# Kernel tuning notes

Measured on AMD Instinct MI355X. Metric: run time of the kernel, lower is better.

Reference implementation:

```python
import jax, jax.numpy as jnp
import numpy as np

ACT_BITS = 8
NUM_HEADS = 6


def weight_quant(w):
    # BitNet b1.58 absmean ternary quantization with straight-through estimator
    scale = 1.0 / jnp.maximum(jnp.mean(jnp.abs(w)), 1e-5)
    wq = jnp.clip(jnp.round(w * scale), -1.0, 1.0) / scale
    return w + jax.lax.stop_gradient(wq - w)


def act_quant(x, bits=ACT_BITS):
    # per-token absmax quantization to `bits` bits, STE
    qb = float(2 ** (bits - 1))
    scale = qb / jnp.maximum(jnp.max(jnp.abs(x), axis=-1, keepdims=True), 1e-5)
    xq = jnp.clip(jnp.round(x * scale), -qb, qb - 1.0) / scale
    return x + jax.lax.stop_gradient(xq - x)


def bitlinear(x, w, b):
    return jnp.einsum('bnc,oc->bno', act_quant(x), weight_quant(w)) + b


def setup_inputs() -> dict:
    key = jax.random.key(0)
    ks = jax.random.split(key, 5)
    B, N, C = 8, 2048, 384
    return {
        'x': jax.random.normal(ks[0], (B, N, C), dtype=jnp.float32),
        'qkv_w': jax.random.normal(ks[1], (3 * C, C), dtype=jnp.float32) * 0.02,
        'qkv_b': jax.random.normal(ks[2], (3 * C,), dtype=jnp.float32) * 0.02,
        'proj_w': jax.random.normal(ks[3], (C, C), dtype=jnp.float32) * 0.02,
        'proj_b': jax.random.normal(ks[4], (C,), dtype=jnp.float32) * 0.02,
    }


def reference(x, qkv_w, qkv_b, proj_w, proj_b):
    B, N, C = x.shape
    H = NUM_HEADS
    D = C // H
    scale = D ** -0.5
    qkv = bitlinear(x, qkv_w, qkv_b)            # [B, N, 3C]
    q, k, v = jnp.split(qkv, 3, axis=-1)
    # [B, H, N, D]
    q = q.reshape(B, N, H, D).transpose(0, 2, 1, 3)
    k = k.reshape(B, N, H, D).transpose(0, 2, 1, 3)
    v = v.reshape(B, N, H, D).transpose(0, 2, 1, 3)
    # full [B, H, N, N] scores in float32, as in the original
    attn = jnp.einsum('bhnd,bhmd->bhnm', q.astype(jnp.float32), k.astype(jnp.float32)) * scale
    attn = jax.nn.softmax(attn, axis=-1).astype(q.dtype)
    out = jnp.einsum('bhnm,bhmd->bhnd', attn, v)
    out = out.transpose(0, 2, 1, 3).reshape(B, N, C)
    return bitlinear(out, proj_w, proj_b)
```

## Files before the change

### kernel.cpp

```cpp
#include <hip/hip_runtime.h>
#include <hip/hip_bf16.h>

typedef short  s16x8  __attribute__((ext_vector_type(8)));
typedef int    i32x4  __attribute__((ext_vector_type(4)));
typedef float  f32x16 __attribute__((ext_vector_type(16)));
typedef unsigned int u32x4 __attribute__((ext_vector_type(4)));
typedef unsigned int u32x2 __attribute__((ext_vector_type(2)));
using u32 = unsigned int;
using u16 = unsigned short;
using as3u = __attribute__((address_space(3))) unsigned int;
using as1u = __attribute__((address_space(1))) unsigned int;

#define FINF __builtin_inff()

constexpr int B_  = 8;
constexpr int N_  = 2048;
constexpr int C_  = 384;
constexpr int H_  = 6;
constexpr int D_  = 64;
constexpr int BN_ = B_ * N_;
constexpr int O3_ = 3 * C_;
constexpr int NW1 = O3_ * C_;
constexpr int NW2 = C_ * C_;
constexpr int BH_ = B_ * H_;

__device__ __forceinline__ u16 f2bf(float f) {
    union { float f; u32 u; } v; v.f = f;
    u32 r = v.u + 0x7FFFu + ((v.u >> 16) & 1u);
    return (u16)(r >> 16);
}
__device__ __forceinline__ float bf2f(u16 u) {
    union { u32 i; float f; } v; v.i = (u32)u << 16; return v.f;
}
__device__ __forceinline__ float exp2a(float x) {
    float r; asm("v_exp_f32 %0, %1" : "=v"(r) : "v"(x)); return r;
}
__device__ __forceinline__ u32 cvtpk(float lo, float hi) {
    u32 r; asm("v_cvt_pk_bf16_f32 %0, %1, %2" : "=v"(r) : "v"(lo), "v"(hi)); return r;
}
__device__ __forceinline__ void plswap(u32& a, u32& b) {
    asm("v_permlane32_swap_b32 %0, %1" : "+v"(a), "+v"(b));
}
__device__ __forceinline__ float max3f(float a, float b, float c) {
    float r; asm("v_max3_f32 %0, %1, %2, %3" : "=v"(r) : "v"(a), "v"(b), "v"(c)); return r;
}
__device__ __forceinline__ u32 pack4i8(float a, float b, float c, float d) {
    int ia = (int)a, ib = (int)b, ic = (int)c, id = (int)d;
    return (u32)(ia & 255) | ((u32)(ib & 255) << 8) | ((u32)(ic & 255) << 16) | ((u32)(id & 255) << 24);
}

__global__ void k_wstats(const float* __restrict__ w1, const float* __restrict__ w2,
                         double* __restrict__ partial) {
    double s1 = 0.0, s2 = 0.0;
    int t = blockIdx.x * 256 + threadIdx.x;
    const int stride = 256 * 256;
    for (int i = t; i < NW1; i += stride) s1 += (double)fabsf(w1[i]);
    for (int i = t; i < NW2; i += stride) s2 += (double)fabsf(w2[i]);
#pragma unroll
    for (int m = 1; m < 64; m <<= 1) { s1 += __shfl_xor(s1, m, 64); s2 += __shfl_xor(s2, m, 64); }
    __shared__ double r1[4], r2[4];
    int wid = threadIdx.x >> 6;
    if ((threadIdx.x & 63) == 0) { r1[wid] = s1; r2[wid] = s2; }
    __syncthreads();
    if (threadIdx.x == 0) {
        partial[2 * blockIdx.x]     = r1[0] + r1[1] + r1[2] + r1[3];
        partial[2 * blockIdx.x + 1] = r2[0] + r2[1] + r2[2] + r2[3];
    }
}

__global__ void k_wfinal(const double* __restrict__ partial, float* __restrict__ scales) {
    int t = threadIdx.x;
    double s1 = partial[2 * t], s2 = partial[2 * t + 1];
#pragma unroll
    for (int m = 1; m < 64; m <<= 1) { s1 += __shfl_xor(s1, m, 64); s2 += __shfl_xor(s2, m, 64); }
    __shared__ double r1[4], r2[4];
    if ((t & 63) == 0) { r1[t >> 6] = s1; r2[t >> 6] = s2; }
    __syncthreads();
    if (t == 0) {
        float m1 = (float)((r1[0] + r1[1] + r1[2] + r1[3]) / (double)NW1);
        float m2 = (float)((r2[0] + r2[1] + r2[2] + r2[3]) / (double)NW2);
        float sc1 = 1.f / fmaxf(m1, 1e-5f);
        float sc2 = 1.f / fmaxf(m2, 1e-5f);
        scales[0] = sc1; scales[1] = 1.f / sc1;
        scales[2] = sc2; scales[3] = 1.f / sc2;
    }
}

__global__ void k_wquant(const float* __restrict__ w1, const float* __restrict__ w2,
                         const float* __restrict__ scales,
                         char* __restrict__ o1, char* __restrict__ o2) {
    float sc1 = scales[0], sc2 = scales[2];
    int t = blockIdx.x * blockDim.x + threadIdx.x;
    int stride = gridDim.x * blockDim.x;
    for (int i = t; i < NW1; i += stride)
        o1[i] = (char)(int)fminf(fmaxf(rintf(w1[i] * sc1), -1.f), 1.f);
    for (int i = t; i < NW2; i += stride)
        o2[i] = (char)(int)fminf(fmaxf(rintf(w2[i] * sc2), -1.f), 1.f);
}

__global__ __launch_bounds__(128) void k_aquant(const float* __restrict__ in,
                                                char* __restrict__ outq,
                                                float* __restrict__ rs) {
    int row = blockIdx.x;
    const float* xr = in + (size_t)row * C_;
    int t = threadIdx.x;
    float4 v = make_float4(0.f, 0.f, 0.f, 0.f);
    if (t < 96) v = ((const float4*)xr)[t];
    float mx = fmaxf(fmaxf(fabsf(v.x), fabsf(v.y)), fmaxf(fabsf(v.z), fabsf(v.w)));
#pragma unroll
    for (int m = 1; m < 64; m <<= 1) mx = fmaxf(mx, __shfl_xor(mx, m, 64));
    __shared__ float red[2];
    if ((t & 63) == 0) red[t >> 6] = mx;
    __syncthreads();
    mx = fmaxf(red[0], red[1]);
    float scale = 128.f / fmaxf(mx, 1e-5f);
    if (t == 0) rs[row] = 1.f / scale;
    if (t < 96) {
        float a = fminf(fmaxf(rintf(v.x * scale), -128.f), 127.f);
        float b = fminf(fmaxf(rintf(v.y * scale), -128.f), 127.f);
        float c = fminf(fmaxf(rintf(v.z * scale), -128.f), 127.f);
        float d = fminf(fmaxf(rintf(v.w * scale), -128.f), 127.f);
        ((u32*)(outq + (size_t)row * C_))[t] = pack4i8(a, b, c, d);
    }
}

__global__ __launch_bounds__(128) void k_caq(const u16* __restrict__ in,
                                             char* __restrict__ outq,
                                             float* __restrict__ rs) {
    int row = blockIdx.x;
    const u16* xr = in + (size_t)row * C_;
    int t = threadIdx.x;
    float4 v = make_float4(0.f, 0.f, 0.f, 0.f);
    if (t < 96) {
        ushort4 u = ((const ushort4*)xr)[t];
        v.x = bf2f(u.x); v.y = bf2f(u.y); v.z = bf2f(u.z); v.w = bf2f(u.w);
    }
    float mx = fmaxf(fmaxf(fabsf(v.x), fabsf(v.y)), fmaxf(fabsf(v.z), fabsf(v.w)));
#pragma unroll
    for (int m = 1; m < 64; m <<= 1) mx = fmaxf(mx, __shfl_xor(mx, m, 64));
    __shared__ float red[2];
    if ((t & 63) == 0) red[t >> 6] = mx;
    __syncthreads();
    mx = fmaxf(red[0], red[1]);
    float scale = 128.f / fmaxf(mx, 1e-5f);
    if (t == 0) rs[row] = 1.f / scale;
    if (t < 96) {
        float a = fminf(fmaxf(rintf(v.x * scale), -128.f), 127.f);
        float b = fminf(fmaxf(rintf(v.y * scale), -128.f), 127.f);
        float c = fminf(fmaxf(rintf(v.z * scale), -128.f), 127.f);
        float d = fminf(fmaxf(rintf(v.w * scale), -128.f), 127.f);
        ((u32*)(outq + (size_t)row * C_))[t] = pack4i8(a, b, c, d);
    }
}

template <int MODE>
__global__ __launch_bounds__(256) void k_gemm(const char* __restrict__ A, const char* __restrict__ W,
                                              const float* __restrict__ rs, const float* __restrict__ scales,
                                              const float* __restrict__ bias,
                                              u16* __restrict__ qg, u16* __restrict__ kg, u16* __restrict__ vtg,
                                              float* __restrict__ fout) {
    constexpr int K = C_;
    __shared__ char As[128 * 128];
    __shared__ char Bs[128 * 128];
    int m0 = blockIdx.x * 128, n0 = blockIdx.y * 128;
    int tid = threadIdx.x, lane = tid & 63, wid = tid >> 6;
    int wm = wid >> 1, wn = wid & 1;

    i32x4 acc[4][4];
#pragma unroll
    for (int a = 0; a < 4; ++a)
#pragma unroll
        for (int b = 0; b < 4; ++b)
#pragma unroll
            for (int r = 0; r < 4; ++r) acc[a][b][r] = 0;

    for (int k0 = 0; k0 < K; k0 += 128) {
#pragma unroll
        for (int t = 0; t < 4; ++t) {
            int P = t * 256 + wid * 64 + lane;
            int row = P >> 3, c8 = (P & 7) ^ (row & 7);
            const char* srcA = A + (size_t)(m0 + row) * K + k0 + c8 * 16;
            const char* srcB = W + (size_t)(n0 + row) * K + k0 + c8 * 16;
            __builtin_amdgcn_global_load_lds((const as1u*)srcA, (as3u*)(As + (size_t)(t * 256 + wid * 64) * 16), 16, 0, 0);
            __builtin_amdgcn_global_load_lds((const as1u*)srcB, (as3u*)(Bs + (size_t)(t * 256 + wid * 64) * 16), 16, 0, 0);
        }
        __syncthreads();
#pragma unroll
        for (int kk = 0; kk < 2; ++kk) {
            i32x4 ar[4], br[4];
#pragma unroll
            for (int f = 0; f < 4; ++f) {
                int rowA = wm * 64 + f * 16 + (lane & 15);
                int rowB = wn * 64 + f * 16 + (lane & 15);
                int cc = kk * 4 + (lane >> 4);
                ar[f] = *(const i32x4*)(&As[(size_t)(rowA * 8 + (cc ^ (rowA & 7))) * 16]);
                br[f] = *(const i32x4*)(&Bs[(size_t)(rowB * 8 + (cc ^ (rowB & 7))) * 16]);
            }
#pragma unroll
            for (int fr = 0; fr < 4; ++fr)
#pragma unroll
                for (int fc = 0; fc < 4; ++fc)
                    acc[fr][fc] = __builtin_amdgcn_mfma_i32_16x16x64_i8(ar[fr], br[fc], acc[fr][fc], 0, 0, 0);
        }
        __syncthreads();
    }

    float rsw = scales[MODE == 0 ? 1 : 3];
    int colg = lane & 15, rowb = (lane >> 4) * 4;
#pragma unroll
    for (int fr = 0; fr < 4; ++fr) {
#pragma unroll
        for (int r = 0; r < 4; ++r) {
            int m = m0 + wm * 64 + fr * 16 + rowb + r;
            float rsm = rs[m] * rsw;
#pragma unroll
            for (int fc = 0; fc < 4; ++fc) {
                int o = n0 + wn * 64 + fc * 16 + colg;
                float val = (float)acc[fr][fc][r] * rsm + bias[o];
                if (MODE == 0) {
                    int b = m >> 11, n = m & 2047;
                    if (o < C_) {
                        int hh = o >> 6, d = o & 63;
                        qg[(size_t)(b * H_ + hh) * (N_ * D_) + n * 64 + d] = f2bf(val * (0.125f * 1.44269504088896f));
                    } else if (o < 2 * C_) {
                        int oo = o - C_; int hh = oo >> 6, d = oo & 63;
                        kg[(size_t)(b * H_ + hh) * (N_ * D_) + n * 64 + d] = f2bf(val);
                    } else {
                        int oo = o - 2 * C_; int hh = oo >> 6, d = oo & 63;
                        vtg[(size_t)(b * H_ + hh) * (N_ * D_) + (size_t)d * N_ + n] = f2bf(val);
                    }
                } else {
                    fout[(size_t)m * C_ + o] = val;
                }
            }
        }
    }
}

__global__ __launch_bounds__(256, 4) void k_flash(const u16* __restrict__ qg, const u16* __restrict__ kg,
                                                  const u16* __restrict__ vtg,
                                                  u16* __restrict__ attno) {
    int i = blockIdx.x;
    int bh = (i & 7) * 6 + ((i >> 3) % 6);
    int qt = (i >> 3) / 6;
    int tid = threadIdx.x;
    int lane = tid & 63;
    int wid = tid >> 6;
    int h = lane >> 5;
    int ql = lane & 31;
    const u16* Qb = qg + (size_t)bh * (N_ * D_);
    const u16* Kb = kg + (size_t)bh * (N_ * D_);
    const u16* Vb = vtg + (size_t)bh * (N_ * D_);
    int q0 = qt * 128 + wid * 32;
    constexpr int NT = N_ / 64;

    __shared__ u16 Ks[2][64 * 64];
    __shared__ u16 Vs[2][64 * 64];

    s16x8 qf[4];
#pragma unroll
    for (int cs = 0; cs < 4; ++cs)
        qf[cs] = *(const s16x8*)(Qb + (size_t)(q0 + ql) * 64 + cs * 16 + h * 8);

    f32x16 od[2];
#pragma unroll
    for (int a = 0; a < 2; ++a)
#pragma unroll
        for (int r = 0; r < 16; ++r) od[a][r] = 0.f;

    float mrun = -FINF;
    float lrun = 0.f;

    auto STAGE = [&](int buf, int t0) {
        int kv0 = t0 * 64;
#pragma unroll
        for (int ii = 0; ii < 2; ++ii) {
            int P = (wid * 2 + ii) * 64 + lane;
            int row = P >> 3, c = (P & 7) ^ (row & 7);
            const u16* srcK = Kb + (size_t)(kv0 + row) * 64 + c * 8;
            __builtin_amdgcn_global_load_lds((const as1u*)srcK,
                (as3u*)(&Ks[buf][(size_t)(wid * 2 + ii) * 64 * 8]), 16, 0, 0);
            const u16* srcV = Vb + (size_t)row * N_ + kv0 + c * 8;
            __builtin_amdgcn_global_load_lds((const as1u*)srcV,
                (as3u*)(&Vs[buf][(size_t)(wid * 2 + ii) * 64 * 8]), 16, 0, 0);
        }
    };

    auto COMPUTE = [&](int buf) {
        f32x16 sA, sB;
#pragma unroll
        for (int r = 0; r < 16; ++r) { sA[r] = 0.f; sB[r] = 0.f; }
        __builtin_amdgcn_s_setprio(1);
#pragma unroll
        for (int cs = 0; cs < 4; ++cs) {
            int slot = (cs * 2 + h) ^ (ql & 7);
            s16x8 kf0 = *(const s16x8*)(&Ks[buf][(size_t)(ql * 8 + slot) * 8]);
            s16x8 kf1 = *(const s16x8*)(&Ks[buf][(size_t)((32 + ql) * 8 + slot) * 8]);
            sA = __builtin_amdgcn_mfma_f32_32x32x16_bf16(kf0, qf[cs], sA, 0, 0, 0);
            sB = __builtin_amdgcn_mfma_f32_32x32x16_bf16(kf1, qf[cs], sB, 0, 0, 0);
        }
        __builtin_amdgcn_s_setprio(0);

        float g0 = max3f(sA[0], sA[1], sA[2]),    g1 = max3f(sA[3], sA[4], sA[5]);
        float g2 = max3f(sA[6], sA[7], sA[8]),    g3 = max3f(sA[9], sA[10], sA[11]);
        float g4 = max3f(sA[12], sA[13], sA[14]), g5 = max3f(sA[15], sB[0], sB[1]);
        float g6 = max3f(sB[2], sB[3], sB[4]),    g7 = max3f(sB[5], sB[6], sB[7]);
        float g8 = max3f(sB[8], sB[9], sB[10]),   g9 = max3f(sB[11], sB[12], sB[13]);
        float g10 = fmaxf(sB[14], sB[15]);
        float h0 = max3f(g0, g1, g2), h1 = max3f(g3, g4, g5), h2 = max3f(g6, g7, g8);
        float mx = fmaxf(max3f(h0, h1, h2), fmaxf(g9, g10));
        mx = fmaxf(mx, __shfl_xor(mx, 32, 64));
        if (!__all(mx <= mrun + 8.f)) {
            float mnew = fmaxf(mrun, mx);
            float fsc = exp2a(mrun - mnew);
            lrun *= fsc;
#pragma unroll
            for (int r = 0; r < 16; ++r) { od[0][r] *= fsc; od[1][r] *= fsc; }
            mrun = mnew;
        }
        float m = mrun;
        float ps0 = 0.f, ps1 = 0.f, ps2 = 0.f, ps3 = 0.f;
#pragma unroll
        for (int r = 0; r < 16; r += 4) {
            float a0 = exp2a(sA[r] - m);     float a1 = exp2a(sA[r + 1] - m);
            float a2 = exp2a(sA[r + 2] - m); float a3 = exp2a(sA[r + 3] - m);
            float b0 = exp2a(sB[r] - m);     float b1 = exp2a(sB[r + 1] - m);
            float b2 = exp2a(sB[r + 2] - m); float b3 = exp2a(sB[r + 3] - m);
            sA[r] = a0; sA[r + 1] = a1; sA[r + 2] = a2; sA[r + 3] = a3;
            sB[r] = b0; sB[r + 1] = b1; sB[r + 2] = b2; sB[r + 3] = b3;
            ps0 += a0 + b0; ps1 += a1 + b1; ps2 += a2 + b2; ps3 += a3 + b3;
        }
        lrun += (ps0 + ps1) + (ps2 + ps3);

#pragma unroll
        for (int sl = 0; sl < 4; ++sl) {
            const int bse = (sl & 1) * 8;
            float p0, p1, p2, p3, p4, p5, p6, p7;
            if (sl < 2) {
                p0 = sA[bse + 0]; p1 = sA[bse + 1]; p2 = sA[bse + 2]; p3 = sA[bse + 3];
                p4 = sA[bse + 4]; p5 = sA[bse + 5]; p6 = sA[bse + 6]; p7 = sA[bse + 7];
            } else {
                p0 = sB[bse + 0]; p1 = sB[bse + 1]; p2 = sB[bse + 2]; p3 = sB[bse + 3];
                p4 = sB[bse + 4]; p5 = sB[bse + 5]; p6 = sB[bse + 6]; p7 = sB[bse + 7];
            }
            u32 A0 = cvtpk(p0, p1);
            u32 A1 = cvtpk(p2, p3);
            u32 B0 = cvtpk(p4, p5);
            u32 B1 = cvtpk(p6, p7);
            plswap(A0, B0);
            plswap(A1, B1);
            u32x4 pw; pw[0] = A0; pw[1] = A1; pw[2] = B0; pw[3] = B1;
            s16x8 pf = __builtin_bit_cast(s16x8, pw);
            __builtin_amdgcn_s_setprio(1);
#pragma unroll
            for (int db = 0; db < 2; ++db) {
                int vrow = db * 32 + ql;
                int slot = (sl * 2 + h) ^ (vrow & 7);
                s16x8 vf = *(const s16x8*)(&Vs[buf][(size_t)(vrow * 8 + slot) * 8]);
                od[db] = __builtin_amdgcn_mfma_f32_32x32x16_bf16(vf, pf, od[db], 0, 0, 0);
            }
            __builtin_amdgcn_s_setprio(0);
        }
    };

    STAGE(0, 0);
    for (int t = 0; t < NT; ++t) {
        if (t + 1 < NT) {
            STAGE((t + 1) & 1, t + 1);
            asm volatile("s_waitcnt vmcnt(4)" ::: "memory");
        } else {
            asm volatile("s_waitcnt vmcnt(0)" ::: "memory");
        }
        __builtin_amdgcn_s_barrier();
        __builtin_amdgcn_sched_barrier(0);
        COMPUTE(t & 1);
        __builtin_amdgcn_sched_barrier(0);
        __builtin_amdgcn_s_barrier();
    }

    {
        float ltot = lrun + __shfl_xor(lrun, 32, 64);
        float inv = 1.f / ltot;
        int bb = bh / H_, head = bh - bb * H_;
        int q = q0 + ql;
        u16* op = attno + ((size_t)(bb * N_ + q)) * C_ + head * 64;
#pragma unroll
        for (int db = 0; db < 2; ++db)
#pragma unroll
            for (int rg = 0; rg < 4; ++rg) {
                int d = db * 32 + 8 * rg + 4 * h;
                u32x2 w;
                w[0] = cvtpk(od[db][rg * 4 + 0] * inv, od[db][rg * 4 + 1] * inv);
                w[1] = cvtpk(od[db][rg * 4 + 2] * inv, od[db][rg * 4 + 3] * inv);
                *(u32x2*)(op + d) = w;
            }
    }
}

extern "C" void kernel_launch(void* const* d_in, const int* in_sizes, int n_in,
                              void* d_out, int out_size, void* d_ws, size_t ws_size,
                              hipStream_t stream) {
    const float* x      = (const float*)d_in[0];
    const float* qkv_w  = (const float*)d_in[1];
    const float* qkv_b  = (const float*)d_in[2];
    const float* proj_w = (const float*)d_in[3];
    const float* proj_b = (const float*)d_in[4];
    float* out = (float*)d_out;

    char* ws = (char*)d_ws;
    size_t off = 0;
    auto alloc = [&](size_t bytes) { size_t p = off; off += (bytes + 255) & ~(size_t)255; return p; };
    double* partial = (double*)(ws + alloc(256 * 2 * sizeof(double)));
    float*  scales  = (float*)(ws + alloc(4 * sizeof(float)));
    char*   wq1     = (char*)(ws + alloc((size_t)NW1));
    char*   wq2     = (char*)(ws + alloc((size_t)NW2));
    char*   xq      = (char*)(ws + alloc((size_t)BN_ * C_));
    float*  rsx     = (float*)(ws + alloc((size_t)BN_ * 4));
    float*  rsa     = (float*)(ws + alloc((size_t)BN_ * 4));
    u16*    qg      = (u16*)(ws + alloc((size_t)BH_ * N_ * D_ * 2));
    u16*    kg      = (u16*)(ws + alloc((size_t)BH_ * N_ * D_ * 2));
    u16*    vtg     = (u16*)(ws + alloc((size_t)BH_ * N_ * D_ * 2));
    u16*    attno   = (u16*)(ws + alloc((size_t)BN_ * C_ * 2));
    (void)ws_size; (void)in_sizes; (void)n_in; (void)out_size;

    k_wstats<<<256, 256, 0, stream>>>(qkv_w, proj_w, partial);
    k_wfinal<<<1, 256, 0, stream>>>(partial, scales);
    k_wquant<<<512, 256, 0, stream>>>(qkv_w, proj_w, scales, wq1, wq2);
    k_aquant<<<BN_, 128, 0, stream>>>(x, xq, rsx);
    k_gemm<0><<<dim3(BN_ / 128, O3_ / 128), 256, 0, stream>>>(xq, wq1, rsx, scales, qkv_b, qg, kg, vtg, nullptr);
    k_flash<<<BH_ * (N_ / 128), 256, 0, stream>>>(qg, kg, vtg, attno);
    k_caq<<<BN_, 128, 0, stream>>>(attno, xq, rsa);
    k_gemm<1><<<dim3(BN_ / 128, C_ / 128), 256, 0, stream>>>(xq, wq2, rsa, scales, proj_b, nullptr, nullptr, nullptr, out);
}
```

Measured before the change: 142.1 us.

## Merge weight-stat and activation-quant prep kernels; fold running max into score init

Combines the weight absmean partial sums and the per-token activation quantization into one launch, and folds the final scale reduction into the weight-quantize kernel. Four small launches become two, which cuts launch gaps and serialization. In the flash kernel, the score accumulators are now initialised with the negated running max, so the MFMA output is already max-shifted and the per-element subtraction before exp is dropped except when the max is rescaled. Every weight-quant block now redundantly reduces the 256 partials, and the running max starts at zero instead of -inf.

```diff
diff --git a/kernel.cpp b/kernel.cpp
--- a/kernel.cpp
+++ b/kernel.cpp
@@ -49,79 +49,77 @@
     return (u32)(ia & 255) | ((u32)(ib & 255) << 8) | ((u32)(ic & 255) << 16) | ((u32)(id & 255) << 24);
 }
 
-__global__ void k_wstats(const float* __restrict__ w1, const float* __restrict__ w2,
-                         double* __restrict__ partial) {
-    double s1 = 0.0, s2 = 0.0;
-    int t = blockIdx.x * 256 + threadIdx.x;
-    const int stride = 256 * 256;
-    for (int i = t; i < NW1; i += stride) s1 += (double)fabsf(w1[i]);
-    for (int i = t; i < NW2; i += stride) s2 += (double)fabsf(w2[i]);
-#pragma unroll
-    for (int m = 1; m < 64; m <<= 1) { s1 += __shfl_xor(s1, m, 64); s2 += __shfl_xor(s2, m, 64); }
+__global__ __launch_bounds__(128) void k_prep(const float* __restrict__ x,
+                                              char* __restrict__ xq, float* __restrict__ rsx,
+                                              const float* __restrict__ w1, const float* __restrict__ w2,
+                                              double* __restrict__ partial) {
+    __shared__ float  redf[2];
+    __shared__ double redd[4];
+    int t = threadIdx.x;
+    if (blockIdx.x < (unsigned)BN_) {
+        int row = blockIdx.x;
+        const float* xr = x + (size_t)row * C_;
+        float4 v = make_float4(0.f, 0.f, 0.f, 0.f);
+        if (t < 96) v = ((const float4*)xr)[t];
+        float mx = fmaxf(fmaxf(fabsf(v.x), fabsf(v.y)), fmaxf(fabsf(v.z), fabsf(v.w)));
+#pragma unroll
+        for (int m = 1; m < 64; m <<= 1) mx = fmaxf(mx, __shfl_xor(mx, m, 64));
+        if ((t & 63) == 0) redf[t >> 6] = mx;
+        __syncthreads();
+        mx = fmaxf(redf[0], redf[1]);
+        float scale = 128.f / fmaxf(mx, 1e-5f);
+        if (t == 0) rsx[row] = 1.f / scale;
+        if (t < 96) {
+            float a = fminf(fmaxf(rintf(v.x * scale), -128.f), 127.f);
+            float b = fminf(fmaxf(rintf(v.y * scale), -128.f), 127.f);
+            float c = fminf(fmaxf(rintf(v.z * scale), -128.f), 127.f);
+            float d = fminf(fmaxf(rintf(v.w * scale), -128.f), 127.f);
+            ((u32*)(xq + (size_t)row * C_))[t] = pack4i8(a, b, c, d);
+        }
+    } else {
+        int b = blockIdx.x - BN_;
+        double s1 = 0.0, s2 = 0.0;
+        int g = b * 128 + t;
+        const int stride = 256 * 128;
+        for (int i = g; i < NW1; i += stride) s1 += (double)fabsf(w1[i]);
+        for (int i = g; i < NW2; i += stride) s2 += (double)fabsf(w2[i]);
+#pragma unroll
+        for (int m = 1; m < 64; m <<= 1) { s1 += __shfl_xor(s1, m, 64); s2 += __shfl_xor(s2, m, 64); }
+        int wid = t >> 6;
+        if ((t & 63) == 0) { redd[wid] = s1; redd[2 + wid] = s2; }
+        __syncthreads();
+        if (t == 0) {
+            partial[2 * b]     = redd[0] + redd[1];
+            partial[2 * b + 1] = redd[2] + redd[3];
+        }
+    }
+}
+
+__global__ __launch_bounds__(256) void k_wqfin(const double* __restrict__ partial,
+                                               const float* __restrict__ w1, const float* __restrict__ w2,
+                                               char* __restrict__ o1, char* __restrict__ o2,
+                                               float* __restrict__ scales) {
     __shared__ double r1[4], r2[4];
-    int wid = threadIdx.x >> 6;
-    if ((threadIdx.x & 63) == 0) { r1[wid] = s1; r2[wid] = s2; }
-    __syncthreads();
-    if (threadIdx.x == 0) {
-        partial[2 * blockIdx.x]     = r1[0] + r1[1] + r1[2] + r1[3];
-        partial[2 * blockIdx.x + 1] = r2[0] + r2[1] + r2[2] + r2[3];
-    }
-}
-
-__global__ void k_wfinal(const double* __restrict__ partial, float* __restrict__ scales) {
     int t = threadIdx.x;
     double s1 = partial[2 * t], s2 = partial[2 * t + 1];
 #pragma unroll
     for (int m = 1; m < 64; m <<= 1) { s1 += __shfl_xor(s1, m, 64); s2 += __shfl_xor(s2, m, 64); }
-    __shared__ double r1[4], r2[4];
     if ((t & 63) == 0) { r1[t >> 6] = s1; r2[t >> 6] = s2; }
     __syncthreads();
-    if (t == 0) {
-        float m1 = (float)((r1[0] + r1[1] + r1[2] + r1[3]) / (double)NW1);
-        float m2 = (float)((r2[0] + r2[1] + r2[2] + r2[3]) / (double)NW2);
-        float sc1 = 1.f / fmaxf(m1, 1e-5f);
-        float sc2 = 1.f / fmaxf(m2, 1e-5f);
+    float m1 = (float)((r1[0] + r1[1] + r1[2] + r1[3]) / (double)NW1);
+    float m2 = (float)((r2[0] + r2[1] + r2[2] + r2[3]) / (double)NW2);
+    float sc1 = 1.f / fmaxf(m1, 1e-5f);
+    float sc2 = 1.f / fmaxf(m2, 1e-5f);
+    if (blockIdx.x == 0 && t == 0) {
         scales[0] = sc1; scales[1] = 1.f / sc1;
         scales[2] = sc2; scales[3] = 1.f / sc2;
     }
-}
-
-__global__ void k_wquant(const float* __restrict__ w1, const float* __restrict__ w2,
-                         const float* __restrict__ scales,
-                         char* __restrict__ o1, char* __restrict__ o2) {
-    float sc1 = scales[0], sc2 = scales[2];
-    int t = blockIdx.x * blockDim.x + threadIdx.x;
-    int stride = gridDim.x * blockDim.x;
-    for (int i = t; i < NW1; i += stride)
+    int g = blockIdx.x * 256 + t;
+    int stride = gridDim.x * 256;
+    for (int i = g; i < NW1; i += stride)
         o1[i] = (char)(int)fminf(fmaxf(rintf(w1[i] * sc1), -1.f), 1.f);
-    for (int i = t; i < NW2; i += stride)
+    for (int i = g; i < NW2; i += stride)
         o2[i] = (char)(int)fminf(fmaxf(rintf(w2[i] * sc2), -1.f), 1.f);
-}
-
-__global__ __launch_bounds__(128) void k_aquant(const float* __restrict__ in,
-                                                char* __restrict__ outq,
-                                                float* __restrict__ rs) {
-    int row = blockIdx.x;
-    const float* xr = in + (size_t)row * C_;
-    int t = threadIdx.x;
-    float4 v = make_float4(0.f, 0.f, 0.f, 0.f);
-    if (t < 96) v = ((const float4*)xr)[t];
-    float mx = fmaxf(fmaxf(fabsf(v.x), fabsf(v.y)), fmaxf(fabsf(v.z), fabsf(v.w)));
-#pragma unroll
-    for (int m = 1; m < 64; m <<= 1) mx = fmaxf(mx, __shfl_xor(mx, m, 64));
-    __shared__ float red[2];
-    if ((t & 63) == 0) red[t >> 6] = mx;
-    __syncthreads();
-    mx = fmaxf(red[0], red[1]);
-    float scale = 128.f / fmaxf(mx, 1e-5f);
-    if (t == 0) rs[row] = 1.f / scale;
-    if (t < 96) {
-        float a = fminf(fmaxf(rintf(v.x * scale), -128.f), 127.f);
-        float b = fminf(fmaxf(rintf(v.y * scale), -128.f), 127.f);
-        float c = fminf(fmaxf(rintf(v.z * scale), -128.f), 127.f);
-        float d = fminf(fmaxf(rintf(v.w * scale), -128.f), 127.f);
-        ((u32*)(outq + (size_t)row * C_))[t] = pack4i8(a, b, c, d);
-    }
 }
 
 __global__ __launch_bounds__(128) void k_caq(const u16* __restrict__ in,
@@ -268,7 +266,7 @@
 #pragma unroll
         for (int r = 0; r < 16; ++r) od[a][r] = 0.f;
 
-    float mrun = -FINF;
+    float mrun = 0.f;
     float lrun = 0.f;
 
     auto STAGE = [&](int buf, int t0) {
@@ -288,8 +286,9 @@
 
     auto COMPUTE = [&](int buf) {
         f32x16 sA, sB;
-#pragma unroll
-        for (int r = 0; r < 16; ++r) { sA[r] = 0.f; sB[r] = 0.f; }
+        float nm = -mrun;
+#pragma unroll
+        for (int r = 0; r < 16; ++r) { sA[r] = nm; sB[r] = nm; }
         __builtin_amdgcn_s_setprio(1);
 #pragma unroll
         for (int cs = 0; cs < 4; ++cs) {
@@ -310,22 +309,23 @@
         float h0 = max3f(g0, g1, g2), h1 = max3f(g3, g4, g5), h2 = max3f(g6, g7, g8);
         float mx = fmaxf(max3f(h0, h1, h2), fmaxf(g9, g10));
         mx = fmaxf(mx, __shfl_xor(mx, 32, 64));
-        if (!__all(mx <= mrun + 8.f)) {
-            float mnew = fmaxf(mrun, mx);
-            float fsc = exp2a(mrun - mnew);
+        if (!__all(mx <= 8.f)) {
+            float delta = fmaxf(mx, 0.f);
+            float fsc = exp2a(-delta);
             lrun *= fsc;
 #pragma unroll
             for (int r = 0; r < 16; ++r) { od[0][r] *= fsc; od[1][r] *= fsc; }
-            mrun = mnew;
-        }
-        float m = mrun;
+            mrun += delta;
+#pragma unroll
+            for (int r = 0; r < 16; ++r) { sA[r] -= delta; sB[r] -= delta; }
+        }
         float ps0 = 0.f, ps1 = 0.f, ps2 = 0.f, ps3 = 0.f;
 #pragma unroll
         for (int r = 0; r < 16; r += 4) {
-            float a0 = exp2a(sA[r] - m);     float a1 = exp2a(sA[r + 1] - m);
-            float a2 = exp2a(sA[r + 2] - m); float a3 = exp2a(sA[r + 3] - m);
-            float b0 = exp2a(sB[r] - m);     float b1 = exp2a(sB[r + 1] - m);
-            float b2 = exp2a(sB[r + 2] - m); float b3 = exp2a(sB[r + 3] - m);
+            float a0 = exp2a(sA[r]);     float a1 = exp2a(sA[r + 1]);
+            float a2 = exp2a(sA[r + 2]); float a3 = exp2a(sA[r + 3]);
+            float b0 = exp2a(sB[r]);     float b1 = exp2a(sB[r + 1]);
+            float b2 = exp2a(sB[r + 2]); float b3 = exp2a(sB[r + 3]);
             sA[r] = a0; sA[r + 1] = a1; sA[r + 2] = a2; sA[r + 3] = a3;
             sB[r] = b0; sB[r + 1] = b1; sB[r + 2] = b2; sB[r + 3] = b3;
             ps0 += a0 + b0; ps1 += a1 + b1; ps2 += a2 + b2; ps3 += a3 + b3;
@@ -423,10 +423,8 @@
     u16*    attno   = (u16*)(ws + alloc((size_t)BN_ * C_ * 2));
     (void)ws_size; (void)in_sizes; (void)n_in; (void)out_size;
 
-    k_wstats<<<256, 256, 0, stream>>>(qkv_w, proj_w, partial);
-    k_wfinal<<<1, 256, 0, stream>>>(partial, scales);
-    k_wquant<<<512, 256, 0, stream>>>(qkv_w, proj_w, scales, wq1, wq2);
-    k_aquant<<<BN_, 128, 0, stream>>>(x, xq, rsx);
+    k_prep<<<BN_ + 256, 128, 0, stream>>>(x, xq, rsx, qkv_w, proj_w, partial);
+    k_wqfin<<<512, 256, 0, stream>>>(partial, qkv_w, proj_w, wq1, wq2, scales);
     k_gemm<0><<<dim3(BN_ / 128, O3_ / 128), 256, 0, stream>>>(xq, wq1, rsx, scales, qkv_b, qg, kg, vtg, nullptr);
     k_flash<<<BH_ * (N_ / 128), 256, 0, stream>>>(qg, kg, vtg, attno);
     k_caq<<<BN_, 128, 0, stream>>>(attno, xq, rsa);
```

Result: no change. 140.5 us (-1.2%).
